# Kernel tuning notes

Hardware: AMD Instinct MI355X
Metric: run time of the kernel (lower is better)

The kernel has to match this reference:

```python
import jax, jax.numpy as jnp
import numpy as np

N = 100000   # total nodes (batched molecules)
E = 250000   # directed edges
B = 2000     # number of graphs
F_IN = 75    # atom feature dim
DIM = 32     # hidden dim


def setup_inputs() -> dict:
    key = jax.random.key(0)
    ks = jax.random.split(key, 12)
    def gl(k, shape, fan_in):
        return (jax.random.normal(k, shape, jnp.float32) / np.sqrt(fan_in)).astype(jnp.float32)
    inp = {}
    inp['node_features'] = jax.random.normal(ks[0], (N, F_IN), jnp.float32)
    inp['edge_features'] = jax.random.normal(ks[1], (E, 11), jnp.float32)
    inp['lin0_w'] = gl(ks[2], (DIM, F_IN), F_IN)
    inp['lin0_b'] = jnp.zeros((DIM,), jnp.float32)
    # edge network: Linear(11,128) -> ReLU -> Linear(128, DIM*DIM)
    inp['nn_w1'] = gl(ks[3], (128, 11), 11)
    inp['nn_b1'] = jnp.zeros((128,), jnp.float32)
    inp['nn_w2'] = gl(ks[4], (DIM * DIM, 128), 128)
    inp['nn_b2'] = jnp.zeros((DIM * DIM,), jnp.float32)
    inp['conv_bias'] = jnp.zeros((DIM,), jnp.float32)  # NNConv bias (root_weight=False)
    # GRU(dim, dim), torch gate order: r, z, n
    inp['gru_wih'] = gl(ks[5], (3 * DIM, DIM), DIM)
    inp['gru_whh'] = gl(ks[6], (3 * DIM, DIM), DIM)
    inp['gru_bih'] = jnp.zeros((3 * DIM,), jnp.float32)
    inp['gru_bhh'] = jnp.zeros((3 * DIM,), jnp.float32)
    # Set2Set LSTM(2*dim, dim), torch gate order: i, f, g, o
    inp['lstm_wih'] = gl(ks[7], (4 * DIM, 2 * DIM), 2 * DIM)
    inp['lstm_whh'] = gl(ks[8], (4 * DIM, DIM), DIM)
    inp['lstm_bih'] = jnp.zeros((4 * DIM,), jnp.float32)
    inp['lstm_bhh'] = jnp.zeros((4 * DIM,), jnp.float32)
    inp['edge_index'] = jax.random.randint(ks[9], (2, E), 0, N)
    inp['graph_index'] = jnp.sort(jax.random.randint(ks[10], (N,), 0, B))
    return inp


def _nnconv(x, edge_w, src, dst, bias):
    # per-edge: gather src features, apply [dim,dim] edge weight, scatter-mean to dst
    msg = jnp.einsum('ei,eio->eo', x[src], edge_w)           # [E, DIM]
    s = jax.ops.segment_sum(msg, dst, num_segments=N)         # [N, DIM]
    cnt = jax.ops.segment_sum(jnp.ones((msg.shape[0],), msg.dtype), dst, num_segments=N)
    mean = s / jnp.maximum(cnt, 1.0)[:, None]
    return mean + bias


def _gru_cell(x, h, wih, whh, bih, bhh):
    gi = x @ wih.T + bih
    gh = h @ whh.T + bhh
    gi_r, gi_z, gi_n = jnp.split(gi, 3, axis=-1)
    gh_r, gh_z, gh_n = jnp.split(gh, 3, axis=-1)
    r = jax.nn.sigmoid(gi_r + gh_r)
    z = jax.nn.sigmoid(gi_z + gh_z)
    n = jnp.tanh(gi_n + r * gh_n)
    return (1.0 - z) * n + z * h


def _lstm_cell(x, h, c, wih, whh, bih, bhh):
    g = x @ wih.T + bih + h @ whh.T + bhh
    i, f, gg, o = jnp.split(g, 4, axis=-1)
    c = jax.nn.sigmoid(f) * c + jax.nn.sigmoid(i) * jnp.tanh(gg)
    h = jax.nn.sigmoid(o) * jnp.tanh(c)
    return h, c


def _set2set(x, batch, wih, whh, bih, bhh, steps=3):
    dim = x.shape[-1]
    h = jnp.zeros((B, dim), x.dtype)
    c = jnp.zeros((B, dim), x.dtype)
    q_star = jnp.zeros((B, 2 * dim), x.dtype)
    for _ in range(steps):
        q, c = _lstm_cell(q_star, h, c, wih, whh, bih, bhh)
        h = q
        e = jnp.sum(x * q[batch], axis=-1)                    # [N]
        emax = jax.ops.segment_max(e, batch, num_segments=B)
        ex = jnp.exp(e - emax[batch])
        denom = jax.ops.segment_sum(ex, batch, num_segments=B)
        a = ex / denom[batch]
        r = jax.ops.segment_sum(a[:, None] * x, batch, num_segments=B)
        q_star = jnp.concatenate([q, r], axis=-1)
    return q_star


def reference(node_features, edge_features, lin0_w, lin0_b, nn_w1, nn_b1, nn_w2, nn_b2,
              conv_bias, gru_wih, gru_whh, gru_bih, gru_bhh,
              lstm_wih, lstm_whh, lstm_bih, lstm_bhh, edge_index, graph_index):
    src, dst = edge_index[0], edge_index[1]
    out = jax.nn.relu(node_features @ lin0_w.T + lin0_b)      # [N, DIM]
    # edge network (edge_features are fixed -> identical every iteration)
    hw = jax.nn.relu(edge_features @ nn_w1.T + nn_b1)
    edge_w = (hw @ nn_w2.T + nn_b2).reshape(-1, DIM, DIM)     # [E, DIM, DIM]
    h = out
    for _ in range(3):
        m = jax.nn.relu(_nnconv(out, edge_w, src, dst, conv_bias))
        h = _gru_cell(m, h, gru_wih, gru_whh, gru_bih, gru_bhh)
        out = h
    pooled = _set2set(out, graph_index, lstm_wih, lstm_whh, lstm_bih, lstm_bhh)
    return pooled, out
```

## Files before the change

kernel.cpp:

```cpp
#include <hip/hip_runtime.h>
#include <stdint.h>

#define N_NODES  100000
#define N_EDGES  250000
#define N_GRAPHS 2000
#define F_IN     75
#define DIM      32
#define H1       128

#define MSG_BLOCKS 977
#define CH        8
#define NSTAGES   17
#define KT_PAD    (CH * NSTAGES)
#define W2F_HALFS (KT_PAD * 1024)

#define CNT_BLOCKS  ((N_EDGES + 255) / 256)
#define OFFS_BLOCKS ((N_NODES + 255) / 256)

typedef _Float16 v8h __attribute__((ext_vector_type(8)));
typedef float    v4f __attribute__((ext_vector_type(4)));

__device__ __forceinline__ void gld_lds16(const void* g, void* l) {
    __builtin_amdgcn_global_load_lds(
        (const __attribute__((address_space(1))) unsigned int*)g,
        (__attribute__((address_space(3))) unsigned int*)l, 16, 0, 0);
}

__global__ __launch_bounds__(256) void lin0_kernel(
    const float* __restrict__ nf, const float* __restrict__ w,
    const float* __restrict__ b, float* __restrict__ h) {
    __shared__ float wl[DIM * F_IN];
    __shared__ float bl[DIM];
    int t = threadIdx.x;
    for (int i = t; i < DIM * F_IN; i += 256) wl[i] = w[i];
    if (t < DIM) bl[t] = b[t];
    __syncthreads();
    int nl = t >> 5, o = t & 31;
    #pragma unroll
    for (int p = 0; p < 4; ++p) {
        int n = blockIdx.x * 32 + p * 8 + nl;
        if (n >= N_NODES) continue;
        const float* row = nf + (size_t)n * F_IN;
        float acc = bl[o];
        #pragma unroll
        for (int i = 0; i < F_IN; ++i) acc += row[i] * wl[o * F_IN + i];
        h[n * DIM + o] = fmaxf(acc, 0.f);
    }
}

__global__ __launch_bounds__(256) void prep_w2f_kernel(
    const float* __restrict__ w2, const float* __restrict__ b2,
    _Float16* __restrict__ w2f) {
    int id = blockIdx.x * 256 + threadIdx.x;
    if (id >= W2F_HALFS) return;
    int j    = id & 7;
    int lane = (id >> 3) & 63;
    int ng   = (id >> 9) & 1;
    int kt   = id >> 10;
    int lr = lane & 15, q = lane >> 4;
    int c = kt * 32 + q * 8 + j;
    int o = ng * 16 + lr;
    float val = 0.f;
    if (c < 4096)      val = w2[((c >> 7) * 32 + o) * H1 + (c & 127)];
    else if (c < 4128) val = b2[(c - 4096) * 32 + o];
    w2f[id] = (_Float16)val;
}

__global__ __launch_bounds__(256) void hw_kernel(
    const float* __restrict__ ef, const float* __restrict__ w1,
    const float* __restrict__ b1, _Float16* __restrict__ hwf,
    int e_off) {
    __shared__ float wl[H1 * 11];
    __shared__ float bl[H1];
    int t = threadIdx.x;
    for (int i = t; i < H1 * 11; i += 256) wl[i] = w1[i];
    if (t < H1) bl[t] = b1[t];
    __syncthreads();
    int k = t & 127;
    #pragma unroll
    for (int p = 0; p < 16; ++p) {
        int le = blockIdx.x * 32 + p * 2 + (t >> 7);
        int e  = e_off + le;
        float acc = 0.f;
        if (e < N_EDGES) {
            const float* row = ef + (size_t)e * 11;
            acc = bl[k];
            #pragma unroll
            for (int i = 0; i < 11; ++i) acc += row[i] * wl[k * 11 + i];
            acc = fmaxf(acc, 0.f);
        }
        size_t addr = (size_t)(le >> 4) * 2048 + (k >> 3) * 128 + (le & 15) * 8 + (k & 7);
        hwf[addr] = (_Float16)acc;
    }
}

__global__ __launch_bounds__(256) void aux_kernel(
    const int* __restrict__ dst, float* __restrict__ cnt,
    const int* __restrict__ gidx, int* __restrict__ gstart) {
    int t = threadIdx.x;
    if (blockIdx.x < CNT_BLOCKS) {
        int e = blockIdx.x * 256 + t;
        if (e < N_EDGES) atomicAdd(&cnt[dst[e]], 1.0f);
    } else {
        int n = (blockIdx.x - CNT_BLOCKS) * 256 + t;
        if (n >= N_NODES) return;
        int b = gidx[n];
        if (n == 0) {
            for (int bb = 0; bb <= b; ++bb) gstart[bb] = 0;
        } else {
            int a = gidx[n - 1];
            for (int bb = a + 1; bb <= b; ++bb) gstart[bb] = n;
        }
        if (n == N_NODES - 1) {
            for (int bb = b + 1; bb <= N_GRAPHS; ++bb) gstart[bb] = N_NODES;
        }
    }
}

__global__ __launch_bounds__(256) void msg_kernel(
    const _Float16* __restrict__ hwf, const _Float16* __restrict__ w2f,
    const float* __restrict__ x, const int* __restrict__ src,
    const int* __restrict__ dst, float* __restrict__ sbuf, int e_off) {
    __shared__ _Float16 xs[32 * 256];
    __shared__ _Float16 bst[2][CH * 1024];

    int t = threadIdx.x;
    int w = t >> 6, lane = t & 63, lr = lane & 15, q = lane >> 4;
    int wbase = w * 64;

    {
        const char* gp = (const char*)w2f;
        char* lp = (char*)&bst[0][0];
        #pragma unroll
        for (int it = 0; it < 4; ++it)
            gld_lds16(gp + it * 4096 + t * 16, lp + it * 4096 + t * 16);
    }

    v8h hwr[4][4];
    {
        const v8h* hv = (const v8h*)hwf;
        int T0 = blockIdx.x * 16 + w * 4;
        #pragma unroll
        for (int mt = 0; mt < 4; ++mt)
            #pragma unroll
            for (int kc = 0; kc < 4; ++kc)
                hwr[mt][kc] = hv[(size_t)(T0 + mt) * 256 + (kc * 4 + q) * 16 + lr];
    }

    {
        int e = e_off + blockIdx.x * 256 + t;
        int ec = e < N_EDGES ? e : N_EDGES - 1;
        int sv = src[ec];
        const float4* xr = (const float4*)(x + (size_t)sv * DIM);
        #pragma unroll
        for (int u = 0; u < 8; ++u) {
            float4 v = xr[u];
            xs[(u * 4 + 0) * 256 + t] = (_Float16)v.x;
            xs[(u * 4 + 1) * 256 + t] = (_Float16)v.y;
            xs[(u * 4 + 2) * 256 + t] = (_Float16)v.z;
            xs[(u * 4 + 3) * 256 + t] = (_Float16)v.w;
        }
    }
    __syncthreads();

    v4f acc[4][2];
    #pragma unroll
    for (int mt = 0; mt < 4; ++mt)
        #pragma unroll
        for (int ng = 0; ng < 2; ++ng) { v4f z = {0.f, 0.f, 0.f, 0.f}; acc[mt][ng] = z; }

    _Float16 xsc[4];

    for (int s = 0; s < NSTAGES - 1; ++s) {
        {
            const char* gp = (const char*)(w2f + (size_t)(s + 1) * CH * 1024);
            char* lp = (char*)&bst[(s + 1) & 1][0];
            #pragma unroll
            for (int it = 0; it < 4; ++it)
                gld_lds16(gp + it * 4096 + t * 16, lp + it * 4096 + t * 16);
        }
        const _Float16* bb = &bst[s & 1][0];
        #pragma unroll
        for (int ktl = 0; ktl < CH; ++ktl) {
            int kt = s * CH + ktl;
            v8h b0 = *(const v8h*)(bb + ktl * 1024 + lane * 8);
            v8h b1 = *(const v8h*)(bb + ktl * 1024 + 512 + lane * 8);
            if ((kt & 3) == 0) {
                int i = kt >> 2;
                #pragma unroll
                for (int mt = 0; mt < 4; ++mt)
                    xsc[mt] = xs[i * 256 + wbase + mt * 16 + lr];
            }
            int kc = kt & 3;
            #pragma unroll
            for (int mt = 0; mt < 4; ++mt) {
                v8h a = hwr[mt][kc] * xsc[mt];
                acc[mt][0] = __builtin_amdgcn_mfma_f32_16x16x32_f16(a, b0, acc[mt][0], 0, 0, 0);
                acc[mt][1] = __builtin_amdgcn_mfma_f32_16x16x32_f16(a, b1, acc[mt][1], 0, 0, 0);
            }
        }
        __syncthreads();
    }
    {
        const _Float16* bb = &bst[0][0];
        v8h b0 = *(const v8h*)(bb + lane * 8);
        v8h b1 = *(const v8h*)(bb + 512 + lane * 8);
        #pragma unroll
        for (int mt = 0; mt < 4; ++mt) {
            v8h a;
            #pragma unroll
            for (int j = 0; j < 8; ++j)
                a[j] = xs[(q * 8 + j) * 256 + wbase + mt * 16 + lr];
            acc[mt][0] = __builtin_amdgcn_mfma_f32_16x16x32_f16(a, b0, acc[mt][0], 0, 0, 0);
            acc[mt][1] = __builtin_amdgcn_mfma_f32_16x16x32_f16(a, b1, acc[mt][1], 0, 0, 0);
        }
    }

    int E0 = e_off + blockIdx.x * 256 + wbase;
    #pragma unroll
    for (int mt = 0; mt < 4; ++mt) {
        #pragma unroll
        for (int r = 0; r < 4; ++r) {
            int e = E0 + mt * 16 + q * 4 + r;
            if (e < N_EDGES) {
                int dv = dst[e];
                float* sp = sbuf + (size_t)dv * DIM;
                atomicAdd(sp + lr,      acc[mt][0][r]);
                atomicAdd(sp + 16 + lr, acc[mt][1][r]);
            }
        }
    }
}

__global__ __launch_bounds__(256) void gru_kernel(
    float* __restrict__ s, const float* __restrict__ cnt,
    const float* __restrict__ cb,
    const float* __restrict__ wih, const float* __restrict__ whh,
    const float* __restrict__ bih, const float* __restrict__ bhh,
    float* __restrict__ h) {
    __shared__ _Float16 wi_l[96 * 40], wh_l[96 * 40];
    __shared__ float bi_l[96], bh_l[96];
    __shared__ _Float16 m_l[64 * 32], h_l[64 * 32];
    int t = threadIdx.x;

    for (int i = t; i < 96 * 32; i += 256) {
        int r = i >> 5, c2 = i & 31;
        wi_l[r * 40 + c2] = (_Float16)wih[i];
        wh_l[r * 40 + c2] = (_Float16)whh[i];
    }
    if (t < 96) { bi_l[t] = bih[t]; bh_l[t] = bhh[t]; }

    {
        int node_l = t >> 2, part = t & 3;
        int n = blockIdx.x * 64 + node_l;
        int nc = n < N_NODES ? n : N_NODES - 1;
        float c = cnt[nc];
        float rc = 1.f / (c > 1.f ? c : 1.f);
        float4* s4 = (float4*)(s + (size_t)nc * DIM + part * 8);
        float4 sa = s4[0], sb = s4[1];
        const float* cbp = cb + part * 8;
        v8h mv;
        mv[0] = (_Float16)fmaxf(sa.x * rc + cbp[0], 0.f);
        mv[1] = (_Float16)fmaxf(sa.y * rc + cbp[1], 0.f);
        mv[2] = (_Float16)fmaxf(sa.z * rc + cbp[2], 0.f);
        mv[3] = (_Float16)fmaxf(sa.w * rc + cbp[3], 0.f);
        mv[4] = (_Float16)fmaxf(sb.x * rc + cbp[4], 0.f);
        mv[5] = (_Float16)fmaxf(sb.y * rc + cbp[5], 0.f);
        mv[6] = (_Float16)fmaxf(sb.z * rc + cbp[6], 0.f);
        mv[7] = (_Float16)fmaxf(sb.w * rc + cbp[7], 0.f);
        *(v8h*)&m_l[node_l * 32 + part * 8] = mv;
        if (n < N_NODES) {
            float4 z4 = {0.f, 0.f, 0.f, 0.f};
            s4[0] = z4; s4[1] = z4;
        }
        const float4* h4 = (const float4*)(h + (size_t)nc * DIM + part * 8);
        float4 ha = h4[0], hb = h4[1];
        v8h hv;
        hv[0] = (_Float16)ha.x; hv[1] = (_Float16)ha.y;
        hv[2] = (_Float16)ha.z; hv[3] = (_Float16)ha.w;
        hv[4] = (_Float16)hb.x; hv[5] = (_Float16)hb.y;
        hv[6] = (_Float16)hb.z; hv[7] = (_Float16)hb.w;
        *(v8h*)&h_l[node_l * 32 + part * 8] = hv;
    }

    __syncthreads();

    int w = t >> 6, lane = t & 63, lr = lane & 15, q = lane >> 4;

    v8h bi6[6], bh6[6];
    v4f ai[6], ah[6];
    #pragma unroll
    for (int nt = 0; nt < 6; ++nt) {
        bi6[nt] = *(const v8h*)&wi_l[(nt * 16 + lr) * 40 + q * 8];
        bh6[nt] = *(const v8h*)&wh_l[(nt * 16 + lr) * 40 + q * 8];
        float bii = bi_l[nt * 16 + lr], bhi = bh_l[nt * 16 + lr];
        v4f ci = {bii, bii, bii, bii}; ai[nt] = ci;
        v4f chh = {bhi, bhi, bhi, bhi}; ah[nt] = chh;
    }

    v8h ma = *(const v8h*)&m_l[(w * 16 + lr) * 32 + q * 8];
    v8h ha = *(const v8h*)&h_l[(w * 16 + lr) * 32 + q * 8];
    #pragma unroll
    for (int nt = 0; nt < 6; ++nt) {
        ai[nt] = __builtin_amdgcn_mfma_f32_16x16x32_f16(ma, bi6[nt], ai[nt], 0, 0, 0);
        ah[nt] = __builtin_amdgcn_mfma_f32_16x16x32_f16(ha, bh6[nt], ah[nt], 0, 0, 0);
    }

    int nb = blockIdx.x * 64 + w * 16 + q * 4;
    #pragma unroll
    for (int g = 0; g < 2; ++g) {
        int o = g * 16 + lr;
        #pragma unroll
        for (int r = 0; r < 4; ++r) {
            int n2 = nb + r;
            if (n2 < N_NODES) {
                float rg = 1.f / (1.f + expf(-(ai[g][r]     + ah[g][r])));
                float zg = 1.f / (1.f + expf(-(ai[2 + g][r] + ah[2 + g][r])));
                float ng = tanhf(ai[4 + g][r] + rg * ah[4 + g][r]);
                float hold = (float)h_l[(w * 16 + q * 4 + r) * 32 + o];
                h[(size_t)n2 * DIM + o] = (1.f - zg) * ng + zg * hold;
            }
        }
    }
}

__global__ __launch_bounds__(256) void s2s_kernel(
    const float* __restrict__ wih, const float* __restrict__ whh,
    const float* __restrict__ bih, const float* __restrict__ bhh,
    float* __restrict__ h, float* __restrict__ c,
    float* __restrict__ rnum, float* __restrict__ denom,
    const float* __restrict__ x, const int* __restrict__ gstart,
    float* __restrict__ outp, int first, int wout) {
    __shared__ float wA[128 * 33], wB[128 * 33], bl[128];
    int t = threadIdx.x;
    for (int i = t; i < 128 * 32; i += 256) {
        int r = i >> 5, cc = i & 31;
        wA[r * 33 + cc] = wih[r * 64 + cc] + whh[r * 32 + cc];
        wB[r * 33 + cc] = wih[r * 64 + 32 + cc];
    }
    if (t < 128) bl[t] = bih[t] + bhh[t];
    __syncthreads();
    int gl = t >> 5, o = t & 31;
    int b = blockIdx.x * 8 + gl;
    if (b >= N_GRAPHS) return;

    float hq = 0.f, rr = 0.f, cv = 0.f;
    if (!first) {
        hq = h[b * DIM + o];
        float d = denom[b];
        rr = d > 0.f ? rnum[b * DIM + o] / d : 0.f;
        cv = c[b * DIM + o];
    }
    float gi = bl[o], gf = bl[32 + o], gg = bl[64 + o], go = bl[96 + o];
    #pragma unroll
    for (int i = 0; i < 32; ++i) {
        float qv = __shfl(hq, i, 32);
        float rv = __shfl(rr, i, 32);
        gi += qv * wA[o * 33 + i]        + rv * wB[o * 33 + i];
        gf += qv * wA[(32 + o) * 33 + i] + rv * wB[(32 + o) * 33 + i];
        gg += qv * wA[(64 + o) * 33 + i] + rv * wB[(64 + o) * 33 + i];
        go += qv * wA[(96 + o) * 33 + i] + rv * wB[(96 + o) * 33 + i];
    }
    float si = 1.f / (1.f + expf(-gi));
    float sf = 1.f / (1.f + expf(-gf));
    float so = 1.f / (1.f + expf(-go));
    float cn = sf * cv + si * tanhf(gg);
    float qo = so * tanhf(cn);
    c[b * DIM + o] = cn;
    h[b * DIM + o] = qo;

    int n0 = gstart[b], n1 = gstart[b + 1];
    float m0 = -3.0e38f, s = 0.f, r = 0.f;
    for (int n = n0; n < n1; ++n) {
        float xo = x[(size_t)n * DIM + o];
        float e = xo * qo;
        #pragma unroll
        for (int mm = 16; mm >= 1; mm >>= 1) e += __shfl_xor(e, mm, 32);
        float nm = fmaxf(m0, e);
        float sc = expf(m0 - nm);
        float ex = expf(e - nm);
        s = s * sc + ex;
        r = r * sc + ex * xo;
        m0 = nm;
    }
    rnum[b * DIM + o] = r;
    if (o == 0) denom[b] = s;
    if (wout) {
        outp[b * 64 + o]      = qo;
        outp[b * 64 + 32 + o] = s > 0.f ? r / s : 0.f;
    }
}

extern "C" void kernel_launch(void* const* d_in, const int* in_sizes, int n_in,
                              void* d_out, int out_size, void* d_ws, size_t ws_size,
                              hipStream_t stream) {
    const float* nf   = (const float*)d_in[0];
    const float* ef   = (const float*)d_in[1];
    const float* l0w  = (const float*)d_in[2];
    const float* l0b  = (const float*)d_in[3];
    const float* w1   = (const float*)d_in[4];
    const float* b1   = (const float*)d_in[5];
    const float* w2   = (const float*)d_in[6];
    const float* b2   = (const float*)d_in[7];
    const float* cb   = (const float*)d_in[8];
    const float* gwih = (const float*)d_in[9];
    const float* gwhh = (const float*)d_in[10];
    const float* gbih = (const float*)d_in[11];
    const float* gbhh = (const float*)d_in[12];
    const float* lwih = (const float*)d_in[13];
    const float* lwhh = (const float*)d_in[14];
    const float* lbih = (const float*)d_in[15];
    const float* lbhh = (const float*)d_in[16];
    const int*   eidx = (const int*)d_in[17];
    const int*   gidx = (const int*)d_in[18];
    const int* src = eidx;
    const int* dst = eidx + N_EDGES;
    float* out = (float*)d_out;
    float* h   = out + (size_t)N_GRAPHS * 64;

    char* ws = (char*)d_ws;
    size_t off = 0;
    auto alloc = [&](size_t bytes) -> void* {
        void* p = ws + off;
        off = (off + bytes + 255) & ~(size_t)255;
        return p;
    };
    float* sbuf  = (float*)alloc((size_t)N_NODES * DIM * 4);
    float* cnt   = (float*)alloc((size_t)N_NODES * 4);
    float* hs    = (float*)alloc((size_t)N_GRAPHS * DIM * 4);
    float* cs    = (float*)alloc((size_t)N_GRAPHS * DIM * 4);
    float* rnum  = (float*)alloc((size_t)N_GRAPHS * DIM * 4);
    float* denom = (float*)alloc((size_t)N_GRAPHS * 4);
    int*   gstart = (int*)alloc((size_t)(N_GRAPHS + 1) * 4);
    _Float16* w2f  = (_Float16*)alloc((size_t)W2F_HALFS * 2);
    size_t fixed = off;
    size_t avail = ws_size > fixed ? ws_size - fixed : 0;

    auto need = [&](int nc) -> size_t {
        int cbk = (MSG_BLOCKS + nc - 1) / nc;
        return (size_t)cbk * 16 * 4096;
    };
    int nchunk = 1;
    while (nchunk < 64 && need(nchunk) > avail) nchunk <<= 1;
    int chunk_blocks = (MSG_BLOCKS + nchunk - 1) / nchunk;
    _Float16* hwf = (_Float16*)alloc(need(nchunk));

    lin0_kernel<<<dim3((N_NODES + 31) / 32), dim3(256), 0, stream>>>(nf, l0w, l0b, h);
    prep_w2f_kernel<<<dim3((W2F_HALFS + 255) / 256), dim3(256), 0, stream>>>(w2, b2, w2f);
    hipMemsetAsync(cnt, 0, (size_t)N_NODES * 4, stream);
    aux_kernel<<<dim3(CNT_BLOCKS + OFFS_BLOCKS), dim3(256), 0, stream>>>(dst, cnt, gidx, gstart);
    if (nchunk == 1) {
        hw_kernel<<<dim3(MSG_BLOCKS * 8), dim3(256), 0, stream>>>(ef, w1, b1, hwf, 0);
    }
    hipMemsetAsync(sbuf, 0, (size_t)N_NODES * DIM * 4, stream);

    for (int it = 0; it < 3; ++it) {
        for (int cix = 0; cix < nchunk; ++cix) {
            int bstart = cix * chunk_blocks;
            int bc = MSG_BLOCKS - bstart;
            if (bc <= 0) break;
            if (bc > chunk_blocks) bc = chunk_blocks;
            int e_off = bstart * 256;
            if (nchunk > 1)
                hw_kernel<<<dim3(bc * 8), dim3(256), 0, stream>>>(ef, w1, b1, hwf, e_off);
            msg_kernel<<<dim3(bc), dim3(256), 0, stream>>>(hwf, w2f, h, src, dst, sbuf, e_off);
        }
        gru_kernel<<<dim3((N_NODES + 63) / 64), dim3(256), 0, stream>>>(
            sbuf, cnt, cb, gwih, gwhh, gbih, gbhh, h);
    }

    for (int st = 0; st < 3; ++st) {
        s2s_kernel<<<dim3((N_GRAPHS + 7) / 8), dim3(256), 0, stream>>>(
            lwih, lwhh, lbih, lbhh, hs, cs, rnum, denom, h, gstart, out,
            st == 0 ? 1 : 0, st == 2 ? 1 : 0);
    }
}
```

Measured before the change: 599.5 us.

## Keep node hidden state in fp16 and preconvert GRU weights once

```diff
diff --git a/kernel.cpp b/kernel.cpp
--- a/kernel.cpp
+++ b/kernel.cpp
@@ -16,6 +16,7 @@
 
 #define CNT_BLOCKS  ((N_EDGES + 255) / 256)
 #define OFFS_BLOCKS ((N_NODES + 255) / 256)
+#define GRUW_BLOCKS 32
 
 typedef _Float16 v8h __attribute__((ext_vector_type(8)));
 typedef float    v4f __attribute__((ext_vector_type(4)));
@@ -28,7 +29,7 @@
 
 __global__ __launch_bounds__(256) void lin0_kernel(
     const float* __restrict__ nf, const float* __restrict__ w,
-    const float* __restrict__ b, float* __restrict__ h) {
+    const float* __restrict__ b, _Float16* __restrict__ h16) {
     __shared__ float wl[DIM * F_IN];
     __shared__ float bl[DIM];
     int t = threadIdx.x;
@@ -44,7 +45,7 @@
         float acc = bl[o];
         #pragma unroll
         for (int i = 0; i < F_IN; ++i) acc += row[i] * wl[o * F_IN + i];
-        h[n * DIM + o] = fmaxf(acc, 0.f);
+        h16[(size_t)n * DIM + o] = (_Float16)fmaxf(acc, 0.f);
     }
 }
 
@@ -96,12 +97,14 @@
 
 __global__ __launch_bounds__(256) void aux_kernel(
     const int* __restrict__ dst, float* __restrict__ cnt,
-    const int* __restrict__ gidx, int* __restrict__ gstart) {
+    const int* __restrict__ gidx, int* __restrict__ gstart,
+    const float* __restrict__ wih, const float* __restrict__ whh,
+    _Float16* __restrict__ gw) {
     int t = threadIdx.x;
     if (blockIdx.x < CNT_BLOCKS) {
         int e = blockIdx.x * 256 + t;
         if (e < N_EDGES) atomicAdd(&cnt[dst[e]], 1.0f);
-    } else {
+    } else if (blockIdx.x < CNT_BLOCKS + OFFS_BLOCKS) {
         int n = (blockIdx.x - CNT_BLOCKS) * 256 + t;
         if (n >= N_NODES) return;
         int b = gidx[n];
@@ -114,12 +117,20 @@
         if (n == N_NODES - 1) {
             for (int bb = b + 1; bb <= N_GRAPHS; ++bb) gstart[bb] = N_NODES;
         }
+    } else {
+        int id = (blockIdx.x - CNT_BLOCKS - OFFS_BLOCKS) * 256 + t;
+        if (id >= 8192) return;
+        int im = id & 4095;
+        int r = im / 40, c = im - r * 40;
+        float val = 0.f;
+        if (r < 96 && c < 32) val = (id < 4096) ? wih[r * 32 + c] : whh[r * 32 + c];
+        gw[id] = (_Float16)val;
     }
 }
 
 __global__ __launch_bounds__(256) void msg_kernel(
     const _Float16* __restrict__ hwf, const _Float16* __restrict__ w2f,
-    const float* __restrict__ x, const int* __restrict__ src,
+    const _Float16* __restrict__ x16, const int* __restrict__ src,
     const int* __restrict__ dst, float* __restrict__ sbuf, int e_off) {
     __shared__ _Float16 xs[32 * 256];
     __shared__ _Float16 bst[2][CH * 1024];
@@ -151,14 +162,13 @@
         int e = e_off + blockIdx.x * 256 + t;
         int ec = e < N_EDGES ? e : N_EDGES - 1;
         int sv = src[ec];
-        const float4* xr = (const float4*)(x + (size_t)sv * DIM);
-        #pragma unroll
-        for (int u = 0; u < 8; ++u) {
-            float4 v = xr[u];
-            xs[(u * 4 + 0) * 256 + t] = (_Float16)v.x;
-            xs[(u * 4 + 1) * 256 + t] = (_Float16)v.y;
-            xs[(u * 4 + 2) * 256 + t] = (_Float16)v.z;
-            xs[(u * 4 + 3) * 256 + t] = (_Float16)v.w;
+        const v8h* xr = (const v8h*)(x16 + (size_t)sv * DIM);
+        #pragma unroll
+        for (int u = 0; u < 4; ++u) {
+            v8h v = xr[u];
+            #pragma unroll
+            for (int j = 0; j < 8; ++j)
+                xs[(u * 8 + j) * 256 + t] = v[j];
         }
     }
     __syncthreads();
@@ -234,53 +244,52 @@
 
 __global__ __launch_bounds__(256) void gru_kernel(
     float* __restrict__ s, const float* __restrict__ cnt,
-    const float* __restrict__ cb,
-    const float* __restrict__ wih, const float* __restrict__ whh,
+    const float* __restrict__ cb, const _Float16* __restrict__ gw,
     const float* __restrict__ bih, const float* __restrict__ bhh,
-    float* __restrict__ h) {
-    __shared__ _Float16 wi_l[96 * 40], wh_l[96 * 40];
+    _Float16* __restrict__ h16, float* __restrict__ hout, int last) {
+    __shared__ _Float16 wi_l[4096], wh_l[4096];
     __shared__ float bi_l[96], bh_l[96];
-    __shared__ _Float16 m_l[64 * 32], h_l[64 * 32];
-    int t = threadIdx.x;
-
-    for (int i = t; i < 96 * 32; i += 256) {
-        int r = i >> 5, c2 = i & 31;
-        wi_l[r * 40 + c2] = (_Float16)wih[i];
-        wh_l[r * 40 + c2] = (_Float16)whh[i];
+    __shared__ _Float16 m_l[128 * 32], h_l[128 * 32];
+    int t = threadIdx.x;
+
+    {
+        const char* gp = (const char*)gw;
+        gld_lds16(gp + t * 16,         (char*)wi_l + t * 16);
+        gld_lds16(gp + 4096 + t * 16,  (char*)wi_l + 4096 + t * 16);
+        gld_lds16(gp + 8192 + t * 16,  (char*)wh_l + t * 16);
+        gld_lds16(gp + 12288 + t * 16, (char*)wh_l + 4096 + t * 16);
     }
     if (t < 96) { bi_l[t] = bih[t]; bh_l[t] = bhh[t]; }
 
     {
-        int node_l = t >> 2, part = t & 3;
-        int n = blockIdx.x * 64 + node_l;
+        int node_l = t >> 1, part = t & 1;
+        int n = blockIdx.x * 128 + node_l;
         int nc = n < N_NODES ? n : N_NODES - 1;
         float c = cnt[nc];
         float rc = 1.f / (c > 1.f ? c : 1.f);
-        float4* s4 = (float4*)(s + (size_t)nc * DIM + part * 8);
-        float4 sa = s4[0], sb = s4[1];
-        const float* cbp = cb + part * 8;
-        v8h mv;
-        mv[0] = (_Float16)fmaxf(sa.x * rc + cbp[0], 0.f);
-        mv[1] = (_Float16)fmaxf(sa.y * rc + cbp[1], 0.f);
-        mv[2] = (_Float16)fmaxf(sa.z * rc + cbp[2], 0.f);
-        mv[3] = (_Float16)fmaxf(sa.w * rc + cbp[3], 0.f);
-        mv[4] = (_Float16)fmaxf(sb.x * rc + cbp[4], 0.f);
-        mv[5] = (_Float16)fmaxf(sb.y * rc + cbp[5], 0.f);
-        mv[6] = (_Float16)fmaxf(sb.z * rc + cbp[6], 0.f);
-        mv[7] = (_Float16)fmaxf(sb.w * rc + cbp[7], 0.f);
-        *(v8h*)&m_l[node_l * 32 + part * 8] = mv;
+        float4* s4 = (float4*)(s + (size_t)nc * DIM + part * 16);
+        const float* cbp = cb + part * 16;
+        #pragma unroll
+        for (int u = 0; u < 2; ++u) {
+            float4 sa = s4[u * 2], sb = s4[u * 2 + 1];
+            v8h mv;
+            mv[0] = (_Float16)fmaxf(sa.x * rc + cbp[u * 8 + 0], 0.f);
+            mv[1] = (_Float16)fmaxf(sa.y * rc + cbp[u * 8 + 1], 0.f);
+            mv[2] = (_Float16)fmaxf(sa.z * rc + cbp[u * 8 + 2], 0.f);
+            mv[3] = (_Float16)fmaxf(sa.w * rc + cbp[u * 8 + 3], 0.f);
+            mv[4] = (_Float16)fmaxf(sb.x * rc + cbp[u * 8 + 4], 0.f);
+            mv[5] = (_Float16)fmaxf(sb.y * rc + cbp[u * 8 + 5], 0.f);
+            mv[6] = (_Float16)fmaxf(sb.z * rc + cbp[u * 8 + 6], 0.f);
+            mv[7] = (_Float16)fmaxf(sb.w * rc + cbp[u * 8 + 7], 0.f);
+            *(v8h*)&m_l[node_l * 32 + part * 16 + u * 8] = mv;
+        }
         if (n < N_NODES) {
             float4 z4 = {0.f, 0.f, 0.f, 0.f};
-            s4[0] = z4; s4[1] = z4;
-        }
-        const float4* h4 = (const float4*)(h + (size_t)nc * DIM + part * 8);
-        float4 ha = h4[0], hb = h4[1];
-        v8h hv;
-        hv[0] = (_Float16)ha.x; hv[1] = (_Float16)ha.y;
-        hv[2] = (_Float16)ha.z; hv[3] = (_Float16)ha.w;
-        hv[4] = (_Float16)hb.x; hv[5] = (_Float16)hb.y;
-        hv[6] = (_Float16)hb.z; hv[7] = (_Float16)hb.w;
-        *(v8h*)&h_l[node_l * 32 + part * 8] = hv;
+            s4[0] = z4; s4[1] = z4; s4[2] = z4; s4[3] = z4;
+        }
+        const v8h* h8 = (const v8h*)(h16 + (size_t)nc * DIM + part * 16);
+        *(v8h*)&h_l[node_l * 32 + part * 16]     = h8[0];
+        *(v8h*)&h_l[node_l * 32 + part * 16 + 8] = h8[1];
     }
 
     __syncthreads();
@@ -288,37 +297,45 @@
     int w = t >> 6, lane = t & 63, lr = lane & 15, q = lane >> 4;
 
     v8h bi6[6], bh6[6];
-    v4f ai[6], ah[6];
     #pragma unroll
     for (int nt = 0; nt < 6; ++nt) {
         bi6[nt] = *(const v8h*)&wi_l[(nt * 16 + lr) * 40 + q * 8];
         bh6[nt] = *(const v8h*)&wh_l[(nt * 16 + lr) * 40 + q * 8];
-        float bii = bi_l[nt * 16 + lr], bhi = bh_l[nt * 16 + lr];
-        v4f ci = {bii, bii, bii, bii}; ai[nt] = ci;
-        v4f chh = {bhi, bhi, bhi, bhi}; ah[nt] = chh;
-    }
-
-    v8h ma = *(const v8h*)&m_l[(w * 16 + lr) * 32 + q * 8];
-    v8h ha = *(const v8h*)&h_l[(w * 16 + lr) * 32 + q * 8];
-    #pragma unroll
-    for (int nt = 0; nt < 6; ++nt) {
-        ai[nt] = __builtin_amdgcn_mfma_f32_16x16x32_f16(ma, bi6[nt], ai[nt], 0, 0, 0);
-        ah[nt] = __builtin_amdgcn_mfma_f32_16x16x32_f16(ha, bh6[nt], ah[nt], 0, 0, 0);
-    }
-
-    int nb = blockIdx.x * 64 + w * 16 + q * 4;
-    #pragma unroll
-    for (int g = 0; g < 2; ++g) {
-        int o = g * 16 + lr;
-        #pragma unroll
-        for (int r = 0; r < 4; ++r) {
-            int n2 = nb + r;
-            if (n2 < N_NODES) {
-                float rg = 1.f / (1.f + expf(-(ai[g][r]     + ah[g][r])));
-                float zg = 1.f / (1.f + expf(-(ai[2 + g][r] + ah[2 + g][r])));
-                float ng = tanhf(ai[4 + g][r] + rg * ah[4 + g][r]);
-                float hold = (float)h_l[(w * 16 + q * 4 + r) * 32 + o];
-                h[(size_t)n2 * DIM + o] = (1.f - zg) * ng + zg * hold;
+    }
+
+    #pragma unroll
+    for (int p = 0; p < 2; ++p) {
+        int tb = w * 32 + p * 16;
+        v4f ai[6], ah[6];
+        #pragma unroll
+        for (int nt = 0; nt < 6; ++nt) {
+            float bii = bi_l[nt * 16 + lr], bhi = bh_l[nt * 16 + lr];
+            v4f ci = {bii, bii, bii, bii}; ai[nt] = ci;
+            v4f chh = {bhi, bhi, bhi, bhi}; ah[nt] = chh;
+        }
+        v8h ma = *(const v8h*)&m_l[(tb + lr) * 32 + q * 8];
+        v8h ha = *(const v8h*)&h_l[(tb + lr) * 32 + q * 8];
+        #pragma unroll
+        for (int nt = 0; nt < 6; ++nt) {
+            ai[nt] = __builtin_amdgcn_mfma_f32_16x16x32_f16(ma, bi6[nt], ai[nt], 0, 0, 0);
+            ah[nt] = __builtin_amdgcn_mfma_f32_16x16x32_f16(ha, bh6[nt], ah[nt], 0, 0, 0);
+        }
+        int nb = blockIdx.x * 128 + tb + q * 4;
+        #pragma unroll
+        for (int g = 0; g < 2; ++g) {
+            int o = g * 16 + lr;
+            #pragma unroll
+            for (int r = 0; r < 4; ++r) {
+                int n2 = nb + r;
+                if (n2 < N_NODES) {
+                    float rg = 1.f / (1.f + expf(-(ai[g][r]     + ah[g][r])));
+                    float zg = 1.f / (1.f + expf(-(ai[2 + g][r] + ah[2 + g][r])));
+                    float ng = tanhf(ai[4 + g][r] + rg * ah[4 + g][r]);
+                    float hold = (float)h_l[(tb + q * 4 + r) * 32 + o];
+                    float hn = (1.f - zg) * ng + zg * hold;
+                    h16[(size_t)n2 * DIM + o] = (_Float16)hn;
+                    if (last) hout[(size_t)n2 * DIM + o] = hn;
+                }
             }
         }
     }
@@ -427,12 +444,14 @@
     };
     float* sbuf  = (float*)alloc((size_t)N_NODES * DIM * 4);
     float* cnt   = (float*)alloc((size_t)N_NODES * 4);
+    _Float16* h16 = (_Float16*)alloc((size_t)N_NODES * DIM * 2);
     float* hs    = (float*)alloc((size_t)N_GRAPHS * DIM * 4);
     float* cs    = (float*)alloc((size_t)N_GRAPHS * DIM * 4);
     float* rnum  = (float*)alloc((size_t)N_GRAPHS * DIM * 4);
     float* denom = (float*)alloc((size_t)N_GRAPHS * 4);
     int*   gstart = (int*)alloc((size_t)(N_GRAPHS + 1) * 4);
     _Float16* w2f  = (_Float16*)alloc((size_t)W2F_HALFS * 2);
+    _Float16* gw   = (_Float16*)alloc((size_t)16384);
     size_t fixed = off;
     size_t avail = ws_size > fixed ? ws_size - fixed : 0;
 
@@ -445,10 +464,11 @@
     int chunk_blocks = (MSG_BLOCKS + nchunk - 1) / nchunk;
     _Float16* hwf = (_Float16*)alloc(need(nchunk));
 
-    lin0_kernel<<<dim3((N_NODES + 31) / 32), dim3(256), 0, stream>>>(nf, l0w, l0b, h);
+    lin0_kernel<<<dim3((N_NODES + 31) / 32), dim3(256), 0, stream>>>(nf, l0w, l0b, h16);
     prep_w2f_kernel<<<dim3((W2F_HALFS + 255) / 256), dim3(256), 0, stream>>>(w2, b2, w2f);
     hipMemsetAsync(cnt, 0, (size_t)N_NODES * 4, stream);
-    aux_kernel<<<dim3(CNT_BLOCKS + OFFS_BLOCKS), dim3(256), 0, stream>>>(dst, cnt, gidx, gstart);
+    aux_kernel<<<dim3(CNT_BLOCKS + OFFS_BLOCKS + GRUW_BLOCKS), dim3(256), 0, stream>>>(
+        dst, cnt, gidx, gstart, gwih, gwhh, gw);
     if (nchunk == 1) {
         hw_kernel<<<dim3(MSG_BLOCKS * 8), dim3(256), 0, stream>>>(ef, w1, b1, hwf, 0);
     }
@@ -463,10 +483,10 @@
             int e_off = bstart * 256;
             if (nchunk > 1)
                 hw_kernel<<<dim3(bc * 8), dim3(256), 0, stream>>>(ef, w1, b1, hwf, e_off);
-            msg_kernel<<<dim3(bc), dim3(256), 0, stream>>>(hwf, w2f, h, src, dst, sbuf, e_off);
-        }
-        gru_kernel<<<dim3((N_NODES + 63) / 64), dim3(256), 0, stream>>>(
-            sbuf, cnt, cb, gwih, gwhh, gbih, gbhh, h);
+            msg_kernel<<<dim3(bc), dim3(256), 0, stream>>>(hwf, w2f, h16, src, dst, sbuf, e_off);
+        }
+        gru_kernel<<<dim3((N_NODES + 127) / 128), dim3(256), 0, stream>>>(
+            sbuf, cnt, cb, gw, gbih, gbhh, h16, h, it == 2 ? 1 : 0);
     }
 
     for (int st = 0; st < 3; ++st) {
```

Measured after the change: 595.9 us. No clear change (-0.6%).
